# Kernel tuning notes

Measured on AMD Instinct MI355X. Metric: run time of the kernel, lower is better.

The kernel has to match this reference:

```python
import jax, jax.numpy as jnp
import numpy as np

B = 16384
D = 1024          # entity_dim
N_LAYERS = 4
TEMPERATURE = 32.0  # sqrt(entity_dim)


def setup_inputs() -> dict:
    key = jax.random.key(0)
    ks = jax.random.split(key, 6)
    d2 = 2 * D
    scale = 1.0 / np.sqrt(d2)
    x1 = jax.random.normal(ks[0], (B, D), dtype=jnp.float32)
    x2 = jax.random.normal(ks[1], (B, D), dtype=jnp.float32)
    # stacked per-layer Linear(2D, 2D) params; torch Linear stores W as [out, in]
    Ws = jax.random.normal(ks[2], (N_LAYERS, d2, d2), dtype=jnp.float32) * scale
    bs = jax.random.normal(ks[3], (N_LAYERS, d2), dtype=jnp.float32) * scale
    W_last = jax.random.normal(ks[4], (D, d2), dtype=jnp.float32) * scale
    b_last = jax.random.normal(ks[5], (D,), dtype=jnp.float32) * scale
    return {"x1": x1, "x2": x2, "Ws": Ws, "bs": bs, "W_last": W_last, "b_last": b_last}


def reference(x1, x2, Ws, bs, W_last, b_last):
    # x: [B, 2, D]
    x = jnp.stack((x1, x2), axis=1)
    # attn: [B, 2, 2] -- tiny self-attention over the 2 tokens
    attn = jnp.einsum('bsd,btd->bst', x / TEMPERATURE, x)
    attn = jax.nn.softmax(attn, axis=-1)  # dropout = identity in eval mode
    x = jnp.einsum('bst,btd->bsd', attn, x)
    # concat the two attended tokens -> [B, 2D]
    h = jnp.concatenate((x[:, 0, :], x[:, 1, :]), axis=-1)
    for i in range(N_LAYERS):
        h = jax.nn.relu(h @ Ws[i].T + bs[i])
    return h @ W_last.T + b_last
```

## Files before the change

### kernel.cpp

```cpp
#include <hip/hip_runtime.h>

typedef __bf16 bf16x8 __attribute__((ext_vector_type(8)));
typedef float f32x4 __attribute__((ext_vector_type(4)));

__device__ __forceinline__ unsigned short f2bf(float f) {
    unsigned int u = __builtin_bit_cast(unsigned int, f);
    u += 0x7FFFu + ((u >> 16) & 1u);
    return (unsigned short)(u >> 16);
}

__global__ void cvt_kernel(const float* __restrict__ in,
                           unsigned short* __restrict__ out, long n4) {
    long i = (long)blockIdx.x * blockDim.x + threadIdx.x;
    long stride = (long)gridDim.x * blockDim.x;
    for (; i < n4; i += stride) {
        float4 v = ((const float4*)in)[i];
        ushort4 o;
        o.x = f2bf(v.x); o.y = f2bf(v.y); o.z = f2bf(v.z); o.w = f2bf(v.w);
        ((ushort4*)out)[i] = o;
    }
}

__global__ __launch_bounds__(256) void attn_kernel(
    const float* __restrict__ x1, const float* __restrict__ x2,
    unsigned short* __restrict__ h) {
    const int D = 1024;
    const int lane = threadIdx.x & 63;
    const int wave = threadIdx.x >> 6;
    const long row = (long)blockIdx.x * 4 + wave;
    const float4* p1 = (const float4*)(x1 + row * D);
    const float4* p2 = (const float4*)(x2 + row * D);
    float4 v1[4], v2[4];
    float s11 = 0.f, s12 = 0.f, s22 = 0.f;
#pragma unroll
    for (int j = 0; j < 4; ++j) {
        v1[j] = p1[lane + 64 * j];
        v2[j] = p2[lane + 64 * j];
        s11 += v1[j].x * v1[j].x + v1[j].y * v1[j].y + v1[j].z * v1[j].z + v1[j].w * v1[j].w;
        s12 += v1[j].x * v2[j].x + v1[j].y * v2[j].y + v1[j].z * v2[j].z + v1[j].w * v2[j].w;
        s22 += v2[j].x * v2[j].x + v2[j].y * v2[j].y + v2[j].z * v2[j].z + v2[j].w * v2[j].w;
    }
#pragma unroll
    for (int off = 1; off < 64; off <<= 1) {
        s11 += __shfl_xor(s11, off);
        s12 += __shfl_xor(s12, off);
        s22 += __shfl_xor(s22, off);
    }
    const float a00 = 1.f / (1.f + expf((s12 - s11) * (1.f / 32.f)));
    const float a10 = 1.f / (1.f + expf((s22 - s12) * (1.f / 32.f)));
    const float a01 = 1.f - a00, a11 = 1.f - a10;
    unsigned short* h0 = h + row * 2048;
#pragma unroll
    for (int j = 0; j < 4; ++j) {
        const int f = lane + 64 * j;
        ushort4 o0, o1;
        o0.x = f2bf(a00 * v1[j].x + a01 * v2[j].x);
        o0.y = f2bf(a00 * v1[j].y + a01 * v2[j].y);
        o0.z = f2bf(a00 * v1[j].z + a01 * v2[j].z);
        o0.w = f2bf(a00 * v1[j].w + a01 * v2[j].w);
        o1.x = f2bf(a10 * v1[j].x + a11 * v2[j].x);
        o1.y = f2bf(a10 * v1[j].y + a11 * v2[j].y);
        o1.z = f2bf(a10 * v1[j].z + a11 * v2[j].z);
        o1.w = f2bf(a10 * v1[j].w + a11 * v2[j].w);
        ((ushort4*)(h0))[f] = o0;
        ((ushort4*)(h0 + 1024))[f] = o1;
    }
}

#define BAR   __builtin_amdgcn_s_barrier()
#define VMW3  asm volatile("s_waitcnt vmcnt(3)" ::: "memory")
#define VMW0  asm volatile("s_waitcnt vmcnt(0)" ::: "memory")
#define PRIO1 __builtin_amdgcn_s_setprio(1)
#define PRIO0 __builtin_amdgcn_s_setprio(0)

template <bool RELU, typename OT>
__global__ __launch_bounds__(512, 4) void gemm128(
    const unsigned short* __restrict__ A,
    const unsigned short* __restrict__ Bw,
    const float* __restrict__ bias,
    OT* __restrict__ C,
    int N, int K) {
    __shared__ __align__(16) unsigned short lds[36864];
    const int tid = threadIdx.x;
    const int lane = tid & 63, wave = tid >> 6;
    const int wm = wave >> 2, wn = wave & 3;
    const int fr = lane & 15, fq = lane >> 4;

    const int cpx = (int)gridDim.x >> 3;
    const int swz = ((int)blockIdx.x & 7) * cpx + ((int)blockIdx.x >> 3);
    const int bm = swz & 127;
    const int bn = swz >> 7;
    const long m0 = (long)bm * 128, n0 = (long)bn * 256;
    const long rowb = (long)K * 2;

    const int flip = ((fr >> 3) & 1) << 5;
    const int lbase = fr * 64 + ((fq * 16) ^ flip);
    const int aRd = wm * 4096 + lbase;
    const int bRd = 8192 + wn * 4096 + lbase;
    const char* ldsc = (const char*)lds;

    const int srow = lane >> 2;
    const int scol = ((lane & 3) << 4) ^ ((lane >> 5) << 5);
    const char* Abl = (const char*)A + m0 * rowb;
    const char* Bbl = (const char*)Bw + n0 * rowb;
    const char* s0 = Abl + (long)(wave * 16 + srow) * rowb + scol;
    const char* s1 = Bbl + (long)(wave * 16 + srow) * rowb + scol;
    const char* s2 = Bbl + (long)(128 + wave * 16 + srow) * rowb + scol;
    const int d0 = wave * 1024 + lane * 16;
    const int d1 = 8192 + wave * 1024 + lane * 16;
    const int d2 = 16384 + wave * 1024 + lane * 16;

    auto gl = [&](const char* src, int dst) {
        __builtin_amdgcn_global_load_lds(
            (const __attribute__((address_space(1))) void*)src,
            (__attribute__((address_space(3))) void*)((char*)lds + dst),
            16, 0, 0);
    };
    auto stage = [&](int kt, int slot) {
        const long ko = (long)kt * 64;
        const int sb = slot * 24576;
        gl(s0 + ko, sb + d0);
        gl(s1 + ko, sb + d1);
        gl(s2 + ko, sb + d2);
    };

    f32x4 acc[4][4] = {};
    bf16x8 Af[4], Bf[4];

    stage(0, 0);
    stage(1, 1);
    VMW3;
    BAR;

    const int NT = K >> 5;
    int sl = 0;
    for (int t = 0; t < NT; ++t) {
        const bool g = (t + 2 < NT);
        if (g) { const int ss = (sl == 0) ? 2 : sl - 1; stage(t + 2, ss); }
        const int sb = sl * 24576;
#pragma unroll
        for (int mq = 0; mq < 4; ++mq)
            Af[mq] = *(const bf16x8*)(ldsc + sb + aRd + mq * 1024);
#pragma unroll
        for (int nf = 0; nf < 4; ++nf)
            Bf[nf] = *(const bf16x8*)(ldsc + sb + bRd + nf * 1024);
        PRIO1;
#pragma unroll
        for (int nf = 0; nf < 4; ++nf)
#pragma unroll
            for (int mq = 0; mq < 4; ++mq)
                acc[mq][nf] = __builtin_amdgcn_mfma_f32_16x16x32_bf16(
                    Bf[nf], Af[mq], acc[mq][nf], 0, 0, 0);
        PRIO0;
        if (g) { VMW3; } else { VMW0; }
        BAR;
        sl = (sl == 2) ? 0 : sl + 1;
    }

    const long crow0 = m0 + wm * 64 + fr;
    const long ccol0 = n0 + wn * 64 + fq * 4;
#pragma unroll
    for (int m = 0; m < 4; ++m) {
        const long rb = (crow0 + m * 16) * N;
#pragma unroll
        for (int n = 0; n < 4; ++n) {
            const float4 bv = *(const float4*)(bias + ccol0 + n * 16);
            float v0 = acc[m][n][0] + bv.x;
            float v1 = acc[m][n][1] + bv.y;
            float v2 = acc[m][n][2] + bv.z;
            float v3 = acc[m][n][3] + bv.w;
            if (RELU) {
                v0 = v0 > 0.f ? v0 : 0.f; v1 = v1 > 0.f ? v1 : 0.f;
                v2 = v2 > 0.f ? v2 : 0.f; v3 = v3 > 0.f ? v3 : 0.f;
            }
            if constexpr (sizeof(OT) == 2) {
                uint2 oo;
                oo.x = (unsigned)f2bf(v0) | ((unsigned)f2bf(v1) << 16);
                oo.y = (unsigned)f2bf(v2) | ((unsigned)f2bf(v3) << 16);
                *(uint2*)((unsigned short*)C + rb + ccol0 + n * 16) = oo;
            } else {
                *(float4*)((float*)C + rb + ccol0 + n * 16) =
                    make_float4(v0, v1, v2, v3);
            }
        }
    }
}

extern "C" void kernel_launch(void* const* d_in, const int* in_sizes, int n_in,
                              void* d_out, int out_size, void* d_ws, size_t ws_size,
                              hipStream_t stream) {
    const float* x1 = (const float*)d_in[0];
    const float* x2 = (const float*)d_in[1];
    const float* Ws = (const float*)d_in[2];
    const float* bs = (const float*)d_in[3];
    const float* Wl = (const float*)d_in[4];
    const float* bl = (const float*)d_in[5];
    float* out = (float*)d_out;

    char* ws = (char*)d_ws;
    unsigned short* hA  = (unsigned short*)(ws);
    unsigned short* hB  = (unsigned short*)(ws + (67108864L));
    unsigned short* Wbf = (unsigned short*)(ws + (134217728L));
    unsigned short* Wlb = (unsigned short*)(ws + (167772160L));

    cvt_kernel<<<2048, 256, 0, stream>>>(Ws, Wbf, 4L * 2048 * 2048 / 4);
    cvt_kernel<<<512, 256, 0, stream>>>(Wl, Wlb, 1024L * 2048 / 4);

    attn_kernel<<<16384 / 4, 256, 0, stream>>>(x1, x2, hA);

    gemm128<true, unsigned short><<<1024, 512, 0, stream>>>(hA, Wbf + 0L * 2048 * 2048, bs + 0 * 2048, hB, 2048, 2048);
    gemm128<true, unsigned short><<<1024, 512, 0, stream>>>(hB, Wbf + 1L * 2048 * 2048, bs + 1 * 2048, hA, 2048, 2048);
    gemm128<true, unsigned short><<<1024, 512, 0, stream>>>(hA, Wbf + 2L * 2048 * 2048, bs + 2 * 2048, hB, 2048, 2048);
    gemm128<true, unsigned short><<<1024, 512, 0, stream>>>(hB, Wbf + 3L * 2048 * 2048, bs + 3 * 2048, hA, 2048, 2048);
    gemm128<false, float><<<512, 512, 0, stream>>>(hA, Wlb, bl, out, 1024, 2048);
}
```

Before: 732.3 us.

## Switch GEMM to 4-wave blocks with 256x128 tiles and larger per-wave fragments

Reshapes the GEMM from 8 waves on a 128x256 tile to 4 waves on a 256x128 tile, so each wave computes a 128x64 output region with 32 accumulators. Staging now issues 6 global-to-LDS loads per thread per k-step, and the wait count is adjusted to match. The aim is to raise MFMA work per LDS fragment read and cut barrier and scheduling overhead per FLOP. The cost is much higher register pressure (64 accumulator vectors plus 12 fragment vectors) and fewer waves to hide latency, which could lower occupancy or cause spills.

```diff
diff --git a/kernel.cpp b/kernel.cpp
--- a/kernel.cpp
+++ b/kernel.cpp
@@ -68,13 +68,13 @@
 }
 
 #define BAR   __builtin_amdgcn_s_barrier()
-#define VMW3  asm volatile("s_waitcnt vmcnt(3)" ::: "memory")
+#define VMW6  asm volatile("s_waitcnt vmcnt(6)" ::: "memory")
 #define VMW0  asm volatile("s_waitcnt vmcnt(0)" ::: "memory")
 #define PRIO1 __builtin_amdgcn_s_setprio(1)
 #define PRIO0 __builtin_amdgcn_s_setprio(0)
 
 template <bool RELU, typename OT>
-__global__ __launch_bounds__(512, 4) void gemm128(
+__global__ __launch_bounds__(256, 2) void gemm4w(
     const unsigned short* __restrict__ A,
     const unsigned short* __restrict__ Bw,
     const float* __restrict__ bias,
@@ -83,32 +83,28 @@
     __shared__ __align__(16) unsigned short lds[36864];
     const int tid = threadIdx.x;
     const int lane = tid & 63, wave = tid >> 6;
-    const int wm = wave >> 2, wn = wave & 3;
+    const int wm = wave >> 1, wn = wave & 1;
     const int fr = lane & 15, fq = lane >> 4;
 
     const int cpx = (int)gridDim.x >> 3;
     const int swz = ((int)blockIdx.x & 7) * cpx + ((int)blockIdx.x >> 3);
-    const int bm = swz & 127;
-    const int bn = swz >> 7;
-    const long m0 = (long)bm * 128, n0 = (long)bn * 256;
+    const int bm = swz & 63;
+    const int bn = swz >> 6;
+    const long m0 = (long)bm * 256, n0 = (long)bn * 128;
     const long rowb = (long)K * 2;
 
     const int flip = ((fr >> 3) & 1) << 5;
     const int lbase = fr * 64 + ((fq * 16) ^ flip);
-    const int aRd = wm * 4096 + lbase;
-    const int bRd = 8192 + wn * 4096 + lbase;
+    const int aRd = wm * 8192 + lbase;
+    const int bRd = 16384 + wn * 4096 + lbase;
     const char* ldsc = (const char*)lds;
 
-    const int srow = lane >> 2;
-    const int scol = ((lane & 3) << 4) ^ ((lane >> 5) << 5);
-    const char* Abl = (const char*)A + m0 * rowb;
-    const char* Bbl = (const char*)Bw + n0 * rowb;
-    const char* s0 = Abl + (long)(wave * 16 + srow) * rowb + scol;
-    const char* s1 = Bbl + (long)(wave * 16 + srow) * rowb + scol;
-    const char* s2 = Bbl + (long)(128 + wave * 16 + srow) * rowb + scol;
-    const int d0 = wave * 1024 + lane * 16;
-    const int d1 = 8192 + wave * 1024 + lane * 16;
-    const int d2 = 16384 + wave * 1024 + lane * 16;
+    const int srow = tid >> 2;
+    const int scol = ((tid & 3) << 4) ^ (((tid >> 5) & 1) << 5);
+    const char* Abl = (const char*)A + m0 * rowb + scol;
+    const char* Bbl = (const char*)Bw + n0 * rowb + scol;
+    const int dA = srow * 64 + (tid & 3) * 16;
+    const int dB = 16384 + srow * 64 + (tid & 3) * 16;
 
     auto gl = [&](const char* src, int dst) {
         __builtin_amdgcn_global_load_lds(
@@ -119,17 +115,20 @@
     auto stage = [&](int kt, int slot) {
         const long ko = (long)kt * 64;
         const int sb = slot * 24576;
-        gl(s0 + ko, sb + d0);
-        gl(s1 + ko, sb + d1);
-        gl(s2 + ko, sb + d2);
+#pragma unroll
+        for (int p = 0; p < 4; ++p)
+            gl(Abl + (long)(p * 64 + srow) * rowb + ko, sb + dA + p * 4096);
+#pragma unroll
+        for (int p = 0; p < 2; ++p)
+            gl(Bbl + (long)(p * 64 + srow) * rowb + ko, sb + dB + p * 4096);
     };
 
-    f32x4 acc[4][4] = {};
-    bf16x8 Af[4], Bf[4];
+    f32x4 acc[8][4] = {};
+    bf16x8 Af[8], Bf[4];
 
     stage(0, 0);
     stage(1, 1);
-    VMW3;
+    VMW6;
     BAR;
 
     const int NT = K >> 5;
@@ -139,7 +138,7 @@
         if (g) { const int ss = (sl == 0) ? 2 : sl - 1; stage(t + 2, ss); }
         const int sb = sl * 24576;
 #pragma unroll
-        for (int mq = 0; mq < 4; ++mq)
+        for (int mq = 0; mq < 8; ++mq)
             Af[mq] = *(const bf16x8*)(ldsc + sb + aRd + mq * 1024);
 #pragma unroll
         for (int nf = 0; nf < 4; ++nf)
@@ -148,19 +147,19 @@
 #pragma unroll
         for (int nf = 0; nf < 4; ++nf)
 #pragma unroll
-            for (int mq = 0; mq < 4; ++mq)
+            for (int mq = 0; mq < 8; ++mq)
                 acc[mq][nf] = __builtin_amdgcn_mfma_f32_16x16x32_bf16(
                     Bf[nf], Af[mq], acc[mq][nf], 0, 0, 0);
         PRIO0;
-        if (g) { VMW3; } else { VMW0; }
+        if (g) { VMW6; } else { VMW0; }
         BAR;
         sl = (sl == 2) ? 0 : sl + 1;
     }
 
-    const long crow0 = m0 + wm * 64 + fr;
+    const long crow0 = m0 + wm * 128 + fr;
     const long ccol0 = n0 + wn * 64 + fq * 4;
 #pragma unroll
-    for (int m = 0; m < 4; ++m) {
+    for (int m = 0; m < 8; ++m) {
         const long rb = (crow0 + m * 16) * N;
 #pragma unroll
         for (int n = 0; n < 4; ++n) {
@@ -208,9 +207,9 @@
 
     attn_kernel<<<16384 / 4, 256, 0, stream>>>(x1, x2, hA);
 
-    gemm128<true, unsigned short><<<1024, 512, 0, stream>>>(hA, Wbf + 0L * 2048 * 2048, bs + 0 * 2048, hB, 2048, 2048);
-    gemm128<true, unsigned short><<<1024, 512, 0, stream>>>(hB, Wbf + 1L * 2048 * 2048, bs + 1 * 2048, hA, 2048, 2048);
-    gemm128<true, unsigned short><<<1024, 512, 0, stream>>>(hA, Wbf + 2L * 2048 * 2048, bs + 2 * 2048, hB, 2048, 2048);
-    gemm128<true, unsigned short><<<1024, 512, 0, stream>>>(hB, Wbf + 3L * 2048 * 2048, bs + 3 * 2048, hA, 2048, 2048);
-    gemm128<false, float><<<512, 512, 0, stream>>>(hA, Wlb, bl, out, 1024, 2048);
-}
+    gemm4w<true, unsigned short><<<1024, 256, 0, stream>>>(hA, Wbf + 0L * 2048 * 2048, bs + 0 * 2048, hB, 2048, 2048);
+    gemm4w<true, unsigned short><<<1024, 256, 0, stream>>>(hB, Wbf + 1L * 2048 * 2048, bs + 1 * 2048, hA, 2048, 2048);
+    gemm4w<true, unsigned short><<<1024, 256, 0, stream>>>(hA, Wbf + 2L * 2048 * 2048, bs + 2 * 2048, hB, 2048, 2048);
+    gemm4w<true, unsigned short><<<1024, 256, 0, stream>>>(hB, Wbf + 3L * 2048 * 2048, bs + 3 * 2048, hA, 2048, 2048);
+    gemm4w<false, float><<<512, 256, 0, stream>>>(hA, Wlb, bl, out, 1024, 2048);
+}
```

Result: slower. 850.1 us (+16.1%).
